# Kernel optimization log

Hardware: AMD Instinct MI355X
Metric: run time of the kernel (lower is better)

## Reference

```python
import jax, jax.numpy as jnp
import numpy as np

N_NODES = 10000
N_GRAPHS = 64
NEG_SLOPE = 0.2
EPS = 1e-16


def gat_conv(x, src, dst, W, a_src, a_dst, bias, heads, out_ch, num_nodes):
    """PyG GATConv (shared lin, add_self_loops already applied to src/dst)."""
    xl = (x @ W).reshape(num_nodes, heads, out_ch)          # [N,H,C]
    alpha_s = jnp.einsum('nhc,hc->nh', xl, a_src)           # [N,H]
    alpha_d = jnp.einsum('nhc,hc->nh', xl, a_dst)           # [N,H]
    e = jax.nn.leaky_relu(alpha_s[src] + alpha_d[dst], NEG_SLOPE)  # [E,H]
    # segment softmax over incoming edges of each destination node
    emax = jax.ops.segment_max(e, dst, num_segments=num_nodes)
    emax = jnp.where(jnp.isfinite(emax), emax, 0.0)
    ee = jnp.exp(e - emax[dst])
    denom = jax.ops.segment_sum(ee, dst, num_segments=num_nodes)
    alpha = ee / (denom[dst] + EPS)                         # [E,H]
    msg = xl[src] * alpha[:, :, None]                       # [E,H,C]
    out = jax.ops.segment_sum(msg, dst, num_segments=num_nodes)  # [N,H,C]
    return out.reshape(num_nodes, heads * out_ch) + bias


def setup_inputs() -> dict:
    key = jax.random.key(0)
    ks = jax.random.split(key, 16)
    H, C, IN = 8, 128, 128
    x = jax.random.normal(ks[0], (N_NODES, IN), jnp.float32)
    edge_index = jax.random.randint(ks[1], (2, 320000), 0, N_NODES, jnp.int64)
    batch = jnp.sort(jax.random.randint(ks[2], (N_NODES,), 0, N_GRAPHS, jnp.int64))
    g = lambda k, shp, fan: jax.random.normal(k, shp, jnp.float32) * (1.0 / np.sqrt(fan))
    return {
        'x': x, 'edge_index': edge_index, 'batch': batch,
        'W1': g(ks[3], (IN, H * C), IN),
        'a_src1': g(ks[4], (H, C), C), 'a_dst1': g(ks[5], (H, C), C),
        'b1': jnp.zeros((H * C,), jnp.float32),
        'W2': g(ks[6], (H * C, C), H * C),
        'a_src2': g(ks[7], (1, C), C), 'a_dst2': g(ks[8], (1, C), C),
        'b2': jnp.zeros((C,), jnp.float32),
        'lin1_w': g(ks[9], (C, 128), C), 'lin1_b': jnp.zeros((128,), jnp.float32),
        'lin2_w': g(ks[10], (128, 1), 128), 'lin2_b': jnp.zeros((1,), jnp.float32),
    }


def reference(x, edge_index, batch, W1, a_src1, a_dst1, b1, W2, a_src2, a_dst2, b2,
              lin1_w, lin1_b, lin2_w, lin2_b):
    loops = jnp.arange(N_NODES, dtype=edge_index.dtype)
    src = jnp.concatenate([edge_index[0], loops])
    dst = jnp.concatenate([edge_index[1], loops])
    h = jax.nn.elu(gat_conv(x, src, dst, W1, a_src1, a_dst1, b1, 8, 128, N_NODES))
    h = jax.nn.elu(gat_conv(h, src, dst, W2, a_src2, a_dst2, b2, 1, 128, N_NODES))
    # global mean pool over graphs
    sums = jax.ops.segment_sum(h, batch, num_segments=N_GRAPHS)
    cnts = jax.ops.segment_sum(jnp.ones((N_NODES,), h.dtype), batch, num_segments=N_GRAPHS)
    pooled = sums / jnp.maximum(cnts, 1.0)[:, None]         # [G,128]
    z = jax.nn.relu(pooled @ lin1_w + lin1_b)
    return (z @ lin2_w + lin2_b).squeeze(1)                 # [G]
```

## Files before the change

kernel.cpp:

```cpp
#include <hip/hip_runtime.h>
#include <math.h>

#define N_NODES 10000
#define N_GRAPHS 64
#define E_RAW 320000
#define E_ALL (E_RAW + N_NODES)
#define NEG_SLOPE 0.2f
#define EPS 1e-16f
#define CAP 192

typedef unsigned short ushort_t;
typedef short short8 __attribute__((ext_vector_type(8)));
typedef float floatx4 __attribute__((ext_vector_type(4)));

static __device__ __forceinline__ float bfl(unsigned u) {
  union { unsigned u; float f; } v; v.u = u << 16; return v.f;
}
static __device__ __forceinline__ float bfh(unsigned u) {
  union { unsigned u; float f; } v; v.u = u & 0xFFFF0000u; return v.f;
}
static __device__ __forceinline__ ushort_t f2bf(float f) {
  union { float f; unsigned u; } v; v.f = f;
  unsigned r = v.u + 0x7FFFu + ((v.u >> 16) & 1u);
  return (ushort_t)(r >> 16);
}

static __device__ __forceinline__ void load16_lds(const ushort_t* gp, ushort_t* ldsbase, int lane) {
#if __has_builtin(__builtin_amdgcn_global_load_lds)
  __builtin_amdgcn_global_load_lds((const __attribute__((address_space(1))) void*)gp,
                                   (__attribute__((address_space(3))) void*)ldsbase, 16, 0, 0);
#else
  *(uint4*)(ldsbase + lane * 8) = *(const uint4*)gp;
#endif
}

static __device__ __forceinline__ void swz_one(const float* __restrict__ W,
                                               ushort_t* __restrict__ Wsw,
                                               int idx, int K, int N) {
  int NT = N >> 4;
  int lane = idx & 63, tile = idx >> 6;
  int nt = tile % NT, kt = tile / NT;
  int n = nt * 16 + (lane & 15);
  int kb = kt * 32 + (lane >> 4) * 8;
  ushort4 lo, hi;
  lo.x = f2bf(W[(size_t)(kb + 0) * N + n]); lo.y = f2bf(W[(size_t)(kb + 1) * N + n]);
  lo.z = f2bf(W[(size_t)(kb + 2) * N + n]); lo.w = f2bf(W[(size_t)(kb + 3) * N + n]);
  hi.x = f2bf(W[(size_t)(kb + 4) * N + n]); hi.y = f2bf(W[(size_t)(kb + 5) * N + n]);
  hi.z = f2bf(W[(size_t)(kb + 6) * N + n]); hi.w = f2bf(W[(size_t)(kb + 7) * N + n]);
  *(ushort4*)(Wsw + (size_t)idx * 8) = lo;
  *(ushort4*)(Wsw + (size_t)idx * 8 + 4) = hi;
}

__global__ __launch_bounds__(1024) void prep_k(const float* __restrict__ x,
                                               const int* __restrict__ batch,
                                               const float* __restrict__ W1,
                                               const float* __restrict__ W2,
                                               ushort_t* __restrict__ xb,
                                               ushort_t* __restrict__ W1sw,
                                               ushort_t* __restrict__ W2sw,
                                               float* __restrict__ zero0,
                                               int* __restrict__ poolcnt) {
  __shared__ int shm[N_GRAPHS];
  const int b = blockIdx.x, t = threadIdx.x;
  if (b < 49) {
    int i4 = b * 1024 + t;
    if (i4 < 49548) *(float4*)(zero0 + i4 * 4) = make_float4(0.f, 0.f, 0.f, 0.f);
  } else if (b == 49) {
    if (t < N_GRAPHS) shm[t] = 0;
    __syncthreads();
    for (int n = t; n < N_NODES; n += 1024) atomicAdd(&shm[batch[n]], 1);
    __syncthreads();
    if (t < N_GRAPHS) poolcnt[t] = shm[t];
  } else if (b < 363) {
    int i4 = (b - 50) * 1024 + t;
    if (i4 < 320000) {
      float4 v = *(const float4*)(x + (size_t)i4 * 4);
      ushort4 o;
      o.x = f2bf(v.x); o.y = f2bf(v.y); o.z = f2bf(v.z); o.w = f2bf(v.w);
      *(ushort4*)(xb + (size_t)i4 * 4) = o;
    }
  } else if (b < 379) {
    int idx = (b - 363) * 1024 + t;
    if (idx < 16384) swz_one(W1, W1sw, idx, 128, 1024);
  } else {
    int idx = (b - 379) * 1024 + t;
    if (idx < 16384) swz_one(W2, W2sw, idx, 1024, 128);
  }
}

__global__ __launch_bounds__(256) void g1f_k(const ushort_t* __restrict__ A,
                                             const ushort_t* __restrict__ Bsw,
                                             ushort_t* __restrict__ Cb,
                                             const float* __restrict__ aS,
                                             const float* __restrict__ aD,
                                             float* __restrict__ asO,
                                             float* __restrict__ adO,
                                             const int* __restrict__ ei,
                                             int* __restrict__ degc,
                                             int* __restrict__ csr) {
  __shared__ ushort_t Albuf[32 * 512];
  __shared__ float epi[4][16][68];
  const int bid = blockIdx.x, t = threadIdx.x;
  if (bid >= 632) {
    int e = (bid - 632) * 256 + t;
    if (e < E_ALL) {
      int s, d;
      if (e < E_RAW) { s = ei[e]; d = ei[E_RAW + e]; }
      else           { s = d = e - E_RAW; }
      int pos = atomicAdd(&degc[d], 1);
      if (pos < CAP) csr[d * CAP + pos] = s;
    }
    return;
  }
  const int M = N_NODES, K = 128, NT = 64;
  const int lane = t & 63, w = t >> 6;
  const int wm = w >> 1, wn = w & 1;
  const int m0 = (bid >> 3) * 128;
  const int n0 = (bid & 7) * 128;
  const int g = lane >> 4, l16 = lane & 15;

  #pragma unroll
  for (int i = 0; i < 8; i++) {
    int tile = w * 8 + i;
    int mtl = tile >> 2, kt = tile & 3;
    int r = m0 + mtl * 16 + l16; r = r < M ? r : M - 1;
    load16_lds(A + (size_t)r * K + kt * 32 + g * 8, &Albuf[tile * 512], lane);
  }
  __syncthreads();

  floatx4 acc[4][4] = {};
  #pragma unroll
  for (int kt = 0; kt < 4; kt++) {
    short8 a[4], b[4];
    #pragma unroll
    for (int mi = 0; mi < 4; mi++)
      a[mi] = *(const short8*)&Albuf[(((wm * 4 + mi) * 4 + kt) * 64 + lane) * 8];
    #pragma unroll
    for (int ni = 0; ni < 4; ni++) {
      int nt = (n0 >> 4) + wn * 4 + ni;
      b[ni] = *(const short8*)(Bsw + ((size_t)(kt * NT + nt) * 64 + lane) * 8);
    }
    #pragma unroll
    for (int mi = 0; mi < 4; mi++)
      #pragma unroll
      for (int ni = 0; ni < 4; ni++)
        acc[mi][ni] = __builtin_amdgcn_mfma_f32_16x16x32_bf16(a[mi], b[ni], acc[mi][ni], 0, 0, 0);
  }

  const int h = bid & 7;
  const int r = lane >> 2, c0 = (lane & 3) * 16;
  const int colh = wn * 64 + c0;
  float asc[16], adc[16];
  #pragma unroll
  for (int c = 0; c < 16; c++) { asc[c] = aS[h * 128 + colh + c]; adc[c] = aD[h * 128 + colh + c]; }
  #pragma unroll
  for (int mi = 0; mi < 4; mi++) {
    #pragma unroll
    for (int ni = 0; ni < 4; ni++)
      #pragma unroll
      for (int reg = 0; reg < 4; reg++)
        epi[w][g * 4 + reg][ni * 16 + l16] = acc[mi][ni][reg];
    float4 v0 = *(float4*)&epi[w][r][c0];
    float4 v1 = *(float4*)&epi[w][r][c0 + 4];
    float4 v2 = *(float4*)&epi[w][r][c0 + 8];
    float4 v3 = *(float4*)&epi[w][r][c0 + 12];
    float vr[16] = {v0.x,v0.y,v0.z,v0.w, v1.x,v1.y,v1.z,v1.w,
                    v2.x,v2.y,v2.z,v2.w, v3.x,v3.y,v3.z,v3.w};
    int grow = m0 + wm * 64 + mi * 16 + r;
    float sp = 0.f, dp = 0.f;
    ushort_t hv[16];
    #pragma unroll
    for (int c = 0; c < 16; c++) {
      sp = fmaf(vr[c], asc[c], sp);
      dp = fmaf(vr[c], adc[c], dp);
      hv[c] = f2bf(vr[c]);
    }
    sp += __shfl_xor(sp, 1); sp += __shfl_xor(sp, 2);
    dp += __shfl_xor(dp, 1); dp += __shfl_xor(dp, 2);
    if (grow < M) {
      uint4 u0, u1;
      u0.x = (unsigned)hv[0] | ((unsigned)hv[1] << 16);
      u0.y = (unsigned)hv[2] | ((unsigned)hv[3] << 16);
      u0.z = (unsigned)hv[4] | ((unsigned)hv[5] << 16);
      u0.w = (unsigned)hv[6] | ((unsigned)hv[7] << 16);
      u1.x = (unsigned)hv[8] | ((unsigned)hv[9] << 16);
      u1.y = (unsigned)hv[10] | ((unsigned)hv[11] << 16);
      u1.z = (unsigned)hv[12] | ((unsigned)hv[13] << 16);
      u1.w = (unsigned)hv[14] | ((unsigned)hv[15] << 16);
      ushort_t* cp = Cb + (size_t)grow * 1024 + (bid & 7) * 128 + wn * 64 + c0;
      *(uint4*)cp = u0;
      *(uint4*)(cp + 8) = u1;
      if ((lane & 3) == 0) {
        atomicAdd(&asO[grow * 8 + h], sp);
        atomicAdd(&adO[grow * 8 + h], dp);
      }
    }
  }
}

__global__ __launch_bounds__(256) void gemm2_k(const ushort_t* __restrict__ A,
                                               const ushort_t* __restrict__ Bsw,
                                               ushort_t* __restrict__ Cb,
                                               const float* __restrict__ aS,
                                               const float* __restrict__ aD,
                                               float* __restrict__ asO,
                                               float* __restrict__ adO) {
  const int M = N_NODES, K = 1024, NT = 8;
  __shared__ ushort_t Albuf[8 * 512];
  __shared__ float epi[4][16][68];
  const int t = threadIdx.x, lane = t & 63, w = t >> 6;
  const int wm = w >> 1, wn = w & 1;
  const int mb0 = blockIdx.x * 32;
  const int g = lane >> 4, l16 = lane & 15;

  floatx4 acc[4] = {};
  for (int ch = 0; ch < 8; ch++) {
    #pragma unroll
    for (int i = 0; i < 2; i++) {
      int tile = w * 2 + i;
      int mtl = tile >> 2, kt = tile & 3;
      int r = mb0 + mtl * 16 + l16; r = r < M ? r : M - 1;
      load16_lds(A + (size_t)r * K + (ch * 4 + kt) * 32 + g * 8, &Albuf[tile * 512], lane);
    }
    __syncthreads();
    #pragma unroll
    for (int ks = 0; ks < 4; ks++) {
      short8 a = *(const short8*)&Albuf[(((wm * 4 + ks)) * 64 + lane) * 8];
      #pragma unroll
      for (int ni = 0; ni < 4; ni++) {
        int nt = wn * 4 + ni, ktg = ch * 4 + ks;
        short8 b = *(const short8*)(Bsw + ((size_t)(ktg * NT + nt) * 64 + lane) * 8);
        acc[ni] = __builtin_amdgcn_mfma_f32_16x16x32_bf16(a, b, acc[ni], 0, 0, 0);
      }
    }
    __syncthreads();
  }

  const int r = lane >> 2, c0 = (lane & 3) * 16;
  const int colh = wn * 64 + c0;
  float asc[16], adc[16];
  #pragma unroll
  for (int c = 0; c < 16; c++) { asc[c] = aS[colh + c]; adc[c] = aD[colh + c]; }
  #pragma unroll
  for (int ni = 0; ni < 4; ni++)
    #pragma unroll
    for (int reg = 0; reg < 4; reg++)
      epi[w][g * 4 + reg][ni * 16 + l16] = acc[ni][reg];
  float4 v0 = *(float4*)&epi[w][r][c0];
  float4 v1 = *(float4*)&epi[w][r][c0 + 4];
  float4 v2 = *(float4*)&epi[w][r][c0 + 8];
  float4 v3 = *(float4*)&epi[w][r][c0 + 12];
  float vr[16] = {v0.x,v0.y,v0.z,v0.w, v1.x,v1.y,v1.z,v1.w,
                  v2.x,v2.y,v2.z,v2.w, v3.x,v3.y,v3.z,v3.w};
  int grow = mb0 + wm * 16 + r;
  float sp = 0.f, dp = 0.f;
  ushort_t hv[16];
  #pragma unroll
  for (int c = 0; c < 16; c++) {
    sp = fmaf(vr[c], asc[c], sp);
    dp = fmaf(vr[c], adc[c], dp);
    hv[c] = f2bf(vr[c]);
  }
  sp += __shfl_xor(sp, 1); sp += __shfl_xor(sp, 2);
  dp += __shfl_xor(dp, 1); dp += __shfl_xor(dp, 2);
  if (grow < M) {
    uint4 u0, u1;
    u0.x = (unsigned)hv[0] | ((unsigned)hv[1] << 16);
    u0.y = (unsigned)hv[2] | ((unsigned)hv[3] << 16);
    u0.z = (unsigned)hv[4] | ((unsigned)hv[5] << 16);
    u0.w = (unsigned)hv[6] | ((unsigned)hv[7] << 16);
    u1.x = (unsigned)hv[8] | ((unsigned)hv[9] << 16);
    u1.y = (unsigned)hv[10] | ((unsigned)hv[11] << 16);
    u1.z = (unsigned)hv[12] | ((unsigned)hv[13] << 16);
    u1.w = (unsigned)hv[14] | ((unsigned)hv[15] << 16);
    ushort_t* cp = Cb + (size_t)grow * 128 + colh;
    *(uint4*)cp = u0;
    *(uint4*)(cp + 8) = u1;
    if ((lane & 3) == 0) {
      atomicAdd(&asO[grow], sp);
      atomicAdd(&adO[grow], dp);
    }
  }
}

__global__ __launch_bounds__(128) void agg1_k(const ushort_t* __restrict__ xlb,
                                              const float* __restrict__ as1,
                                              const float* __restrict__ ad1,
                                              const float* __restrict__ b1,
                                              const int* __restrict__ degc,
                                              const int* __restrict__ csr,
                                              ushort_t* __restrict__ out) {
  int dst = blockIdx.x, t = threadIdx.x;
  int deg = degc[dst]; deg = deg < CAP ? deg : CAP;
  int beg = dst * CAP;
  __shared__ int ss[CAP];
  __shared__ float alE[CAP][8];
  __shared__ float sred[8][17];
  __shared__ float mh[8], sh[8];
  for (int e = t; e < deg; e += 128) ss[e] = csr[beg + e];
  __syncthreads();
  int h2 = t & 7, slot = t >> 3;
  float adh2 = ad1[dst * 8 + h2];
  float pm = -1e30f;
  for (int e = slot; e < deg; e += 16) {
    float v = as1[ss[e] * 8 + h2] + adh2;
    v = v > 0.f ? v : NEG_SLOPE * v;
    alE[e][h2] = v;
    pm = fmaxf(pm, v);
  }
  sred[h2][slot] = pm;
  __syncthreads();
  if (t < 8) {
    float m = sred[t][0];
    for (int i = 1; i < 16; i++) m = fmaxf(m, sred[t][i]);
    mh[t] = m;
  }
  __syncthreads();
  float m2 = mh[h2];
  float ps = 0.f;
  for (int e = slot; e < deg; e += 16) ps += __expf(alE[e][h2] - m2);
  sred[h2][slot] = ps;
  __syncthreads();
  if (t < 8) {
    float s = 0.f;
    for (int i = 0; i < 16; i++) s += sred[t][i];
    sh[t] = 1.0f / (s + EPS);
  }
  __syncthreads();
  float inv2 = sh[h2];
  for (int e = slot; e < deg; e += 16) alE[e][h2] = __expf(alE[e][h2] - m2) * inv2;
  __syncthreads();
  int h = t >> 4;
  float acc[8] = {};
  const ushort_t* xp = xlb + 8 * t;
  #pragma unroll 4
  for (int e = 0; e < deg; e++) {
    float a = alE[e][h];
    const uint4 u = *(const uint4*)(xp + (size_t)ss[e] * 1024);
    acc[0] = fmaf(a, bfl(u.x), acc[0]); acc[1] = fmaf(a, bfh(u.x), acc[1]);
    acc[2] = fmaf(a, bfl(u.y), acc[2]); acc[3] = fmaf(a, bfh(u.y), acc[3]);
    acc[4] = fmaf(a, bfl(u.z), acc[4]); acc[5] = fmaf(a, bfh(u.z), acc[5]);
    acc[6] = fmaf(a, bfl(u.w), acc[6]); acc[7] = fmaf(a, bfh(u.w), acc[7]);
  }
  ushort_t hv[8];
  #pragma unroll
  for (int j = 0; j < 8; j++) {
    int o = 8 * t + j;
    float v = acc[j] + b1[o];
    v = v > 0.f ? v : (expf(v) - 1.0f);
    hv[j] = f2bf(v);
  }
  uint4 up;
  up.x = (unsigned)hv[0] | ((unsigned)hv[1] << 16);
  up.y = (unsigned)hv[2] | ((unsigned)hv[3] << 16);
  up.z = (unsigned)hv[4] | ((unsigned)hv[5] << 16);
  up.w = (unsigned)hv[6] | ((unsigned)hv[7] << 16);
  *(uint4*)(out + (size_t)dst * 1024 + 8 * t) = up;
}

__global__ __launch_bounds__(64) void agg2_k(const ushort_t* __restrict__ xlb2,
                                             const float* __restrict__ as2,
                                             const float* __restrict__ ad2,
                                             const float* __restrict__ b2,
                                             const int* __restrict__ degc,
                                             const int* __restrict__ csr,
                                             const int* __restrict__ batch,
                                             float* __restrict__ poolsum) {
  int dst = blockIdx.x, t = threadIdx.x;
  int deg = degc[dst]; deg = deg < CAP ? deg : CAP;
  int beg = dst * CAP;
  float adv = ad2[dst];
  __shared__ int ss[CAP];
  __shared__ float al[CAP];
  for (int e = t; e < deg; e += 64) ss[e] = csr[beg + e];
  __syncthreads();
  float pm = -1e30f;
  for (int e = t; e < deg; e += 64) {
    float v = as2[ss[e]] + adv;
    v = v > 0.f ? v : NEG_SLOPE * v;
    al[e] = v;
    pm = fmaxf(pm, v);
  }
  #pragma unroll
  for (int off = 32; off; off >>= 1) pm = fmaxf(pm, __shfl_xor(pm, off));
  float m = pm;
  float ps = 0.f;
  for (int e = t; e < deg; e += 64) ps += __expf(al[e] - m);
  #pragma unroll
  for (int off = 32; off; off >>= 1) ps += __shfl_xor(ps, off);
  float inv = 1.0f / (ps + EPS);
  for (int e = t; e < deg; e += 64) al[e] = __expf(al[e] - m) * inv;
  __syncthreads();
  float acc0 = 0.f, acc1 = 0.f;
  const ushort_t* xp = xlb2 + 2 * t;
  #pragma unroll 4
  for (int e = 0; e < deg; e++) {
    unsigned u = *(const unsigned*)(xp + (size_t)ss[e] * 128);
    acc0 = fmaf(al[e], bfl(u), acc0);
    acc1 = fmaf(al[e], bfh(u), acc1);
  }
  int c0 = 2 * t;
  float v0 = acc0 + b2[c0];
  float v1 = acc1 + b2[c0 + 1];
  v0 = v0 > 0.f ? v0 : (expf(v0) - 1.0f);
  v1 = v1 > 0.f ? v1 : (expf(v1) - 1.0f);
  int g = batch[dst];
  atomicAdd(&poolsum[g * 128 + c0], v0);
  atomicAdd(&poolsum[g * 128 + c0 + 1], v1);
}

__global__ __launch_bounds__(128) void final_k(const float* __restrict__ poolsum,
                                               const int* __restrict__ cnt,
                                               const float* __restrict__ l1w,
                                               const float* __restrict__ l1b,
                                               const float* __restrict__ l2w,
                                               const float* __restrict__ l2b,
                                               float* __restrict__ out) {
  int g = blockIdx.x, t = threadIdx.x;
  __shared__ float pooled[128];
  float c = fmaxf((float)cnt[g], 1.0f);
  pooled[t] = poolsum[g * 128 + t] / c;
  __syncthreads();
  float acc = l1b[t];
  for (int i = 0; i < 128; i++) acc = fmaf(pooled[i], l1w[i * 128 + t], acc);
  acc = fmaxf(acc, 0.0f);
  float p = acc * l2w[t];
  #pragma unroll
  for (int off = 32; off; off >>= 1) p += __shfl_down(p, off);
  __shared__ float r[2];
  if ((t & 63) == 0) r[t >> 6] = p;
  __syncthreads();
  if (t == 0) out[g] = r[0] + r[1] + l2b[0];
}

extern "C" void kernel_launch(void* const* d_in, const int* in_sizes, int n_in,
                              void* d_out, int out_size, void* d_ws, size_t ws_size,
                              hipStream_t stream) {
  const float* x    = (const float*)d_in[0];
  const int*   ei   = (const int*)d_in[1];
  const int*   batch= (const int*)d_in[2];
  const float* W1   = (const float*)d_in[3];
  const float* aS1  = (const float*)d_in[4];
  const float* aD1  = (const float*)d_in[5];
  const float* b1   = (const float*)d_in[6];
  const float* W2   = (const float*)d_in[7];
  const float* aS2  = (const float*)d_in[8];
  const float* aD2  = (const float*)d_in[9];
  const float* b2   = (const float*)d_in[10];
  const float* l1w  = (const float*)d_in[11];
  const float* l1b  = (const float*)d_in[12];
  const float* l2w  = (const float*)d_in[13];
  const float* l2b  = (const float*)d_in[14];
  float* out = (float*)d_out;

  ushort_t* xlb1   = (ushort_t*)d_ws;
  ushort_t* h1b    = xlb1 + 10240000;
  ushort_t* xlb2   = h1b + 10240000;
  ushort_t* xb     = xlb2 + 1280000;
  ushort_t* W1sw   = xb + 1280000;
  ushort_t* W2sw   = W1sw + 131072;
  float*    zero0  = (float*)(W2sw + 131072);
  float*    as1    = zero0;
  float*    ad1    = as1 + 80000;
  float*    as2    = ad1 + 80000;
  float*    ad2    = as2 + 10000;
  float*    poolsum= ad2 + 10000;
  int*      degc   = (int*)(poolsum + 8192);
  int*      poolcnt= degc + 10000;
  int*      csr    = poolcnt + 64;

  prep_k<<<395, 1024, 0, stream>>>(x, batch, W1, W2, xb, W1sw, W2sw, zero0, poolcnt);
  g1f_k<<<632 + 1290, 256, 0, stream>>>(xb, W1sw, xlb1, aS1, aD1, as1, ad1, ei, degc, csr);
  agg1_k<<<N_NODES, 128, 0, stream>>>(xlb1, as1, ad1, b1, degc, csr, h1b);
  gemm2_k<<<313, 256, 0, stream>>>(h1b, W2sw, xlb2, aS2, aD2, as2, ad2);
  agg2_k<<<N_NODES, 64, 0, stream>>>(xlb2, as2, ad2, b2, degc, csr, batch, poolsum);
  final_k<<<N_GRAPHS, 128, 0, stream>>>(poolsum, poolcnt, l1w, l1b, l2w, l2b, out);
}
```

Baseline: 259.5 us.

## Fuse all stages into one persistent kernel with software grid barriers

Replaces six kernel launches with one persistent kernel of 512 blocks that runs prep, GEMM1, aggregation 1, GEMM2, aggregation 2 and the final MLP in sequence, separated by atomic-counter grid barriers. Zeroing moves to a hipMemsetAsync. Aggregation blocks now handle two or four destination nodes each, so all stages fit in a fixed 256-thread block. This removes launch gaps and tail effects between stages. In exchange it assumes all 512 blocks are co-resident (a deadlock risk otherwise), adds barrier spin cost, and gives up the per-kernel block shapes and occupancy tuning.

```diff
diff --git a/kernel.cpp b/kernel.cpp
--- a/kernel.cpp
+++ b/kernel.cpp
@@ -8,6 +8,7 @@
 #define NEG_SLOPE 0.2f
 #define EPS 1e-16f
 #define CAP 192
+#define NBLK 512
 
 typedef unsigned short ushort_t;
 typedef short short8 __attribute__((ext_vector_type(8)));
@@ -51,74 +52,29 @@
   *(ushort4*)(Wsw + (size_t)idx * 8 + 4) = hi;
 }
 
-__global__ __launch_bounds__(1024) void prep_k(const float* __restrict__ x,
-                                               const int* __restrict__ batch,
-                                               const float* __restrict__ W1,
-                                               const float* __restrict__ W2,
-                                               ushort_t* __restrict__ xb,
-                                               ushort_t* __restrict__ W1sw,
-                                               ushort_t* __restrict__ W2sw,
-                                               float* __restrict__ zero0,
-                                               int* __restrict__ poolcnt) {
-  __shared__ int shm[N_GRAPHS];
-  const int b = blockIdx.x, t = threadIdx.x;
-  if (b < 49) {
-    int i4 = b * 1024 + t;
-    if (i4 < 49548) *(float4*)(zero0 + i4 * 4) = make_float4(0.f, 0.f, 0.f, 0.f);
-  } else if (b == 49) {
-    if (t < N_GRAPHS) shm[t] = 0;
-    __syncthreads();
-    for (int n = t; n < N_NODES; n += 1024) atomicAdd(&shm[batch[n]], 1);
-    __syncthreads();
-    if (t < N_GRAPHS) poolcnt[t] = shm[t];
-  } else if (b < 363) {
-    int i4 = (b - 50) * 1024 + t;
-    if (i4 < 320000) {
-      float4 v = *(const float4*)(x + (size_t)i4 * 4);
-      ushort4 o;
-      o.x = f2bf(v.x); o.y = f2bf(v.y); o.z = f2bf(v.z); o.w = f2bf(v.w);
-      *(ushort4*)(xb + (size_t)i4 * 4) = o;
-    }
-  } else if (b < 379) {
-    int idx = (b - 363) * 1024 + t;
-    if (idx < 16384) swz_one(W1, W1sw, idx, 128, 1024);
-  } else {
-    int idx = (b - 379) * 1024 + t;
-    if (idx < 16384) swz_one(W2, W2sw, idx, 1024, 128);
-  }
-}
-
-__global__ __launch_bounds__(256) void g1f_k(const ushort_t* __restrict__ A,
-                                             const ushort_t* __restrict__ Bsw,
-                                             ushort_t* __restrict__ Cb,
-                                             const float* __restrict__ aS,
-                                             const float* __restrict__ aD,
-                                             float* __restrict__ asO,
-                                             float* __restrict__ adO,
-                                             const int* __restrict__ ei,
-                                             int* __restrict__ degc,
-                                             int* __restrict__ csr) {
-  __shared__ ushort_t Albuf[32 * 512];
-  __shared__ float epi[4][16][68];
-  const int bid = blockIdx.x, t = threadIdx.x;
-  if (bid >= 632) {
-    int e = (bid - 632) * 256 + t;
-    if (e < E_ALL) {
-      int s, d;
-      if (e < E_RAW) { s = ei[e]; d = ei[E_RAW + e]; }
-      else           { s = d = e - E_RAW; }
-      int pos = atomicAdd(&degc[d], 1);
-      if (pos < CAP) csr[d * CAP + pos] = s;
-    }
-    return;
-  }
+static __device__ __forceinline__ void gbar(int* cnt) {
+  __syncthreads();
+  if (threadIdx.x == 0) {
+    __hip_atomic_fetch_add(cnt, 1, __ATOMIC_ACQ_REL, __HIP_MEMORY_SCOPE_AGENT);
+    while (__hip_atomic_load(cnt, __ATOMIC_ACQUIRE, __HIP_MEMORY_SCOPE_AGENT) < NBLK)
+      __builtin_amdgcn_s_sleep(2);
+  }
+  __syncthreads();
+}
+
+static __device__ __forceinline__ void gemm1_tile(int v, char* shraw,
+    const ushort_t* __restrict__ A, const ushort_t* __restrict__ Bsw,
+    ushort_t* __restrict__ Cb, const float* __restrict__ aS,
+    const float* __restrict__ aD, float* __restrict__ asO, float* __restrict__ adO) {
+  ushort_t* Albuf = (ushort_t*)shraw;
+  float (*epi)[16][68] = (float (*)[16][68])shraw;
+  const int t = threadIdx.x, lane = t & 63, w = t >> 6;
+  const int wm = w >> 1, wn = w & 1;
+  const int m0 = (v >> 3) * 128;
+  const int h = v & 7;
+  const int g = lane >> 4, l16 = lane & 15;
   const int M = N_NODES, K = 128, NT = 64;
-  const int lane = t & 63, w = t >> 6;
-  const int wm = w >> 1, wn = w & 1;
-  const int m0 = (bid >> 3) * 128;
-  const int n0 = (bid & 7) * 128;
-  const int g = lane >> 4, l16 = lane & 15;
-
+  __syncthreads();
   #pragma unroll
   for (int i = 0; i < 8; i++) {
     int tile = w * 8 + i;
@@ -127,7 +83,6 @@
     load16_lds(A + (size_t)r * K + kt * 32 + g * 8, &Albuf[tile * 512], lane);
   }
   __syncthreads();
-
   floatx4 acc[4][4] = {};
   #pragma unroll
   for (int kt = 0; kt < 4; kt++) {
@@ -137,7 +92,7 @@
       a[mi] = *(const short8*)&Albuf[(((wm * 4 + mi) * 4 + kt) * 64 + lane) * 8];
     #pragma unroll
     for (int ni = 0; ni < 4; ni++) {
-      int nt = (n0 >> 4) + wn * 4 + ni;
+      int nt = h * 8 + wn * 4 + ni;
       b[ni] = *(const short8*)(Bsw + ((size_t)(kt * NT + nt) * 64 + lane) * 8);
     }
     #pragma unroll
@@ -146,8 +101,7 @@
       for (int ni = 0; ni < 4; ni++)
         acc[mi][ni] = __builtin_amdgcn_mfma_f32_16x16x32_bf16(a[mi], b[ni], acc[mi][ni], 0, 0, 0);
   }
-
-  const int h = bid & 7;
+  __syncthreads();
   const int r = lane >> 2, c0 = (lane & 3) * 16;
   const int colh = wn * 64 + c0;
   float asc[16], adc[16];
@@ -187,7 +141,7 @@
       u1.y = (unsigned)hv[10] | ((unsigned)hv[11] << 16);
       u1.z = (unsigned)hv[12] | ((unsigned)hv[13] << 16);
       u1.w = (unsigned)hv[14] | ((unsigned)hv[15] << 16);
-      ushort_t* cp = Cb + (size_t)grow * 1024 + (bid & 7) * 128 + wn * 64 + c0;
+      ushort_t* cp = Cb + (size_t)grow * 1024 + h * 128 + wn * 64 + c0;
       *(uint4*)cp = u0;
       *(uint4*)(cp + 8) = u1;
       if ((lane & 3) == 0) {
@@ -198,21 +152,17 @@
   }
 }
 
-__global__ __launch_bounds__(256) void gemm2_k(const ushort_t* __restrict__ A,
-                                               const ushort_t* __restrict__ Bsw,
-                                               ushort_t* __restrict__ Cb,
-                                               const float* __restrict__ aS,
-                                               const float* __restrict__ aD,
-                                               float* __restrict__ asO,
-                                               float* __restrict__ adO) {
-  const int M = N_NODES, K = 1024, NT = 8;
-  __shared__ ushort_t Albuf[8 * 512];
-  __shared__ float epi[4][16][68];
+static __device__ __forceinline__ void gemm2_tile(int v, char* shraw,
+    const ushort_t* __restrict__ A, const ushort_t* __restrict__ Bsw,
+    ushort_t* __restrict__ Cb, const float* __restrict__ aS,
+    const float* __restrict__ aD, float* __restrict__ asO, float* __restrict__ adO) {
+  ushort_t* Albuf = (ushort_t*)shraw;
+  float (*epi)[16][68] = (float (*)[16][68])(shraw + 8192);
   const int t = threadIdx.x, lane = t & 63, w = t >> 6;
   const int wm = w >> 1, wn = w & 1;
-  const int mb0 = blockIdx.x * 32;
+  const int mb0 = v * 32;
   const int g = lane >> 4, l16 = lane & 15;
-
+  const int M = N_NODES, K = 1024, NT = 8;
   floatx4 acc[4] = {};
   for (int ch = 0; ch < 8; ch++) {
     #pragma unroll
@@ -235,7 +185,6 @@
     }
     __syncthreads();
   }
-
   const int r = lane >> 2, c0 = (lane & 3) * 16;
   const int colh = wn * 64 + c0;
   float asc[16], adc[16];
@@ -281,62 +230,60 @@
       atomicAdd(&adO[grow], dp);
     }
   }
-}
-
-__global__ __launch_bounds__(128) void agg1_k(const ushort_t* __restrict__ xlb,
-                                              const float* __restrict__ as1,
-                                              const float* __restrict__ ad1,
-                                              const float* __restrict__ b1,
-                                              const int* __restrict__ degc,
-                                              const int* __restrict__ csr,
-                                              ushort_t* __restrict__ out) {
-  int dst = blockIdx.x, t = threadIdx.x;
+  __syncthreads();
+}
+
+static __device__ __forceinline__ void agg1_pair(int p, char* shraw,
+    const ushort_t* __restrict__ xlb, const float* __restrict__ as1,
+    const float* __restrict__ ad1, const float* __restrict__ b1,
+    const int* __restrict__ degc, const int* __restrict__ csr,
+    ushort_t* __restrict__ out) {
+  struct Sh { int ss[CAP]; float alE[CAP][8]; float sred[8][17]; float mh[8]; float sh[8]; };
+  const int t = threadIdx.x, half = t >> 7, th = t & 127;
+  Sh* S = ((Sh*)shraw) + half;
+  const int dst = 2 * p + half;
   int deg = degc[dst]; deg = deg < CAP ? deg : CAP;
-  int beg = dst * CAP;
-  __shared__ int ss[CAP];
-  __shared__ float alE[CAP][8];
-  __shared__ float sred[8][17];
-  __shared__ float mh[8], sh[8];
-  for (int e = t; e < deg; e += 128) ss[e] = csr[beg + e];
-  __syncthreads();
-  int h2 = t & 7, slot = t >> 3;
+  const int beg = dst * CAP;
+  for (int e = th; e < deg; e += 128) S->ss[e] = csr[beg + e];
+  __syncthreads();
+  const int h2 = th & 7, slot = th >> 3;
   float adh2 = ad1[dst * 8 + h2];
   float pm = -1e30f;
   for (int e = slot; e < deg; e += 16) {
-    float v = as1[ss[e] * 8 + h2] + adh2;
+    float v = as1[S->ss[e] * 8 + h2] + adh2;
     v = v > 0.f ? v : NEG_SLOPE * v;
-    alE[e][h2] = v;
+    S->alE[e][h2] = v;
     pm = fmaxf(pm, v);
   }
-  sred[h2][slot] = pm;
-  __syncthreads();
-  if (t < 8) {
-    float m = sred[t][0];
-    for (int i = 1; i < 16; i++) m = fmaxf(m, sred[t][i]);
-    mh[t] = m;
-  }
-  __syncthreads();
-  float m2 = mh[h2];
+  S->sred[h2][slot] = pm;
+  __syncthreads();
+  if (th < 8) {
+    float m = S->sred[th][0];
+    for (int i = 1; i < 16; i++) m = fmaxf(m, S->sred[th][i]);
+    S->mh[th] = m;
+  }
+  __syncthreads();
+  float m2 = S->mh[h2];
   float ps = 0.f;
-  for (int e = slot; e < deg; e += 16) ps += __expf(alE[e][h2] - m2);
-  sred[h2][slot] = ps;
-  __syncthreads();
-  if (t < 8) {
+  for (int e = slot; e < deg; e += 16) ps += __expf(S->alE[e][h2] - m2);
+  S->sred[h2][slot] = ps;
+  __syncthreads();
+  if (th < 8) {
     float s = 0.f;
-    for (int i = 0; i < 16; i++) s += sred[t][i];
-    sh[t] = 1.0f / (s + EPS);
-  }
-  __syncthreads();
-  float inv2 = sh[h2];
-  for (int e = slot; e < deg; e += 16) alE[e][h2] = __expf(alE[e][h2] - m2) * inv2;
-  __syncthreads();
-  int h = t >> 4;
+    for (int i = 0; i < 16; i++) s += S->sred[th][i];
+    S->sh[th] = 1.0f / (s + EPS);
+  }
+  __syncthreads();
+  float inv2 = S->sh[h2];
+  for (int e = slot; e < deg; e += 16) S->alE[e][h2] = __expf(S->alE[e][h2] - m2) * inv2;
+  __syncthreads();
+  const int h = th >> 4;
   float acc[8] = {};
-  const ushort_t* xp = xlb + 8 * t;
+  const ushort_t* xp = xlb + 8 * th;
   #pragma unroll 4
   for (int e = 0; e < deg; e++) {
-    float a = alE[e][h];
-    const uint4 u = *(const uint4*)(xp + (size_t)ss[e] * 1024);
+    float a = S->alE[e][h];
+    const uint4 u = *(const uint4*)(xp + (size_t)S->ss[e] * 1024);
     acc[0] = fmaf(a, bfl(u.x), acc[0]); acc[1] = fmaf(a, bfh(u.x), acc[1]);
     acc[2] = fmaf(a, bfl(u.y), acc[2]); acc[3] = fmaf(a, bfh(u.y), acc[3]);
     acc[4] = fmaf(a, bfl(u.z), acc[4]); acc[5] = fmaf(a, bfh(u.z), acc[5]);
@@ -345,7 +292,7 @@
   ushort_t hv[8];
   #pragma unroll
   for (int j = 0; j < 8; j++) {
-    int o = 8 * t + j;
+    int o = 8 * th + j;
     float v = acc[j] + b1[o];
     v = v > 0.f ? v : (expf(v) - 1.0f);
     hv[j] = f2bf(v);
@@ -355,51 +302,48 @@
   up.y = (unsigned)hv[2] | ((unsigned)hv[3] << 16);
   up.z = (unsigned)hv[4] | ((unsigned)hv[5] << 16);
   up.w = (unsigned)hv[6] | ((unsigned)hv[7] << 16);
-  *(uint4*)(out + (size_t)dst * 1024 + 8 * t) = up;
-}
-
-__global__ __launch_bounds__(64) void agg2_k(const ushort_t* __restrict__ xlb2,
-                                             const float* __restrict__ as2,
-                                             const float* __restrict__ ad2,
-                                             const float* __restrict__ b2,
-                                             const int* __restrict__ degc,
-                                             const int* __restrict__ csr,
-                                             const int* __restrict__ batch,
-                                             float* __restrict__ poolsum) {
-  int dst = blockIdx.x, t = threadIdx.x;
+  *(uint4*)(out + (size_t)dst * 1024 + 8 * th) = up;
+  __syncthreads();
+}
+
+static __device__ __forceinline__ void agg2_quad(int q, char* shraw,
+    const ushort_t* __restrict__ xlb2, const float* __restrict__ as2,
+    const float* __restrict__ ad2, const float* __restrict__ b2,
+    const int* __restrict__ degc, const int* __restrict__ csr,
+    const int* __restrict__ batch, float* __restrict__ poolsum) {
+  struct Sh { int ss[CAP]; float al[CAP]; };
+  const int t = threadIdx.x, qt = t >> 6, l = t & 63;
+  Sh* S = ((Sh*)shraw) + qt;
+  const int dst = 4 * q + qt;
   int deg = degc[dst]; deg = deg < CAP ? deg : CAP;
-  int beg = dst * CAP;
+  const int beg = dst * CAP;
   float adv = ad2[dst];
-  __shared__ int ss[CAP];
-  __shared__ float al[CAP];
-  for (int e = t; e < deg; e += 64) ss[e] = csr[beg + e];
-  __syncthreads();
+  for (int e = l; e < deg; e += 64) S->ss[e] = csr[beg + e];
   float pm = -1e30f;
-  for (int e = t; e < deg; e += 64) {
-    float v = as2[ss[e]] + adv;
+  for (int e = l; e < deg; e += 64) {
+    float v = as2[S->ss[e]] + adv;
     v = v > 0.f ? v : NEG_SLOPE * v;
-    al[e] = v;
+    S->al[e] = v;
     pm = fmaxf(pm, v);
   }
   #pragma unroll
   for (int off = 32; off; off >>= 1) pm = fmaxf(pm, __shfl_xor(pm, off));
   float m = pm;
   float ps = 0.f;
-  for (int e = t; e < deg; e += 64) ps += __expf(al[e] - m);
+  for (int e = l; e < deg; e += 64) ps += __expf(S->al[e] - m);
   #pragma unroll
   for (int off = 32; off; off >>= 1) ps += __shfl_xor(ps, off);
   float inv = 1.0f / (ps + EPS);
-  for (int e = t; e < deg; e += 64) al[e] = __expf(al[e] - m) * inv;
-  __syncthreads();
+  for (int e = l; e < deg; e += 64) S->al[e] = __expf(S->al[e] - m) * inv;
   float acc0 = 0.f, acc1 = 0.f;
-  const ushort_t* xp = xlb2 + 2 * t;
+  const ushort_t* xp = xlb2 + 2 * l;
   #pragma unroll 4
   for (int e = 0; e < deg; e++) {
-    unsigned u = *(const unsigned*)(xp + (size_t)ss[e] * 128);
-    acc0 = fmaf(al[e], bfl(u), acc0);
-    acc1 = fmaf(al[e], bfh(u), acc1);
-  }
-  int c0 = 2 * t;
+    unsigned u = *(const unsigned*)(xp + (size_t)S->ss[e] * 128);
+    acc0 = fmaf(S->al[e], bfl(u), acc0);
+    acc1 = fmaf(S->al[e], bfh(u), acc1);
+  }
+  int c0 = 2 * l;
   float v0 = acc0 + b2[c0];
   float v1 = acc1 + b2[c0 + 1];
   v0 = v0 > 0.f ? v0 : (expf(v0) - 1.0f);
@@ -409,28 +353,85 @@
   atomicAdd(&poolsum[g * 128 + c0 + 1], v1);
 }
 
-__global__ __launch_bounds__(128) void final_k(const float* __restrict__ poolsum,
-                                               const int* __restrict__ cnt,
-                                               const float* __restrict__ l1w,
-                                               const float* __restrict__ l1b,
-                                               const float* __restrict__ l2w,
-                                               const float* __restrict__ l2b,
-                                               float* __restrict__ out) {
-  int g = blockIdx.x, t = threadIdx.x;
-  __shared__ float pooled[128];
+static __device__ __forceinline__ void final_half(char* shraw,
+    const float* __restrict__ poolsum, const int* __restrict__ cnt,
+    const float* __restrict__ l1w, const float* __restrict__ l1b,
+    const float* __restrict__ l2w, const float* __restrict__ l2b,
+    float* __restrict__ out) {
+  struct Sh { float pooled[128]; float r[2]; };
+  const int t = threadIdx.x, half = t >> 7, th = t & 127;
+  Sh* F = ((Sh*)shraw) + half;
+  const int g = blockIdx.x * 2 + half;
   float c = fmaxf((float)cnt[g], 1.0f);
-  pooled[t] = poolsum[g * 128 + t] / c;
-  __syncthreads();
-  float acc = l1b[t];
-  for (int i = 0; i < 128; i++) acc = fmaf(pooled[i], l1w[i * 128 + t], acc);
+  F->pooled[th] = poolsum[g * 128 + th] / c;
+  __syncthreads();
+  float acc = l1b[th];
+  for (int i = 0; i < 128; i++) acc = fmaf(F->pooled[i], l1w[i * 128 + th], acc);
   acc = fmaxf(acc, 0.0f);
-  float p = acc * l2w[t];
+  float p = acc * l2w[th];
   #pragma unroll
   for (int off = 32; off; off >>= 1) p += __shfl_down(p, off);
-  __shared__ float r[2];
-  if ((t & 63) == 0) r[t >> 6] = p;
-  __syncthreads();
-  if (t == 0) out[g] = r[0] + r[1] + l2b[0];
+  if ((th & 63) == 0) F->r[th >> 6] = p;
+  __syncthreads();
+  if (th == 0) out[g] = F->r[0] + F->r[1] + l2b[0];
+}
+
+__global__ __launch_bounds__(256, 2) void mega_k(
+    const float* __restrict__ x, const int* __restrict__ ei,
+    const int* __restrict__ batch,
+    const float* __restrict__ W1, const float* __restrict__ aS1,
+    const float* __restrict__ aD1, const float* __restrict__ b1,
+    const float* __restrict__ W2, const float* __restrict__ aS2,
+    const float* __restrict__ aD2, const float* __restrict__ b2,
+    const float* __restrict__ l1w, const float* __restrict__ l1b,
+    const float* __restrict__ l2w, const float* __restrict__ l2b,
+    ushort_t* xb, ushort_t* W1sw, ushort_t* W2sw,
+    ushort_t* xlb1, ushort_t* h1b, ushort_t* xlb2,
+    float* as1, float* ad1, float* as2, float* ad2,
+    float* poolsum, int* poolcnt, int* degc, int* csr, int* bar,
+    float* out) {
+  __shared__ __align__(16) char shraw[32768];
+  const int bid = blockIdx.x, t = threadIdx.x;
+  const int gtid = bid * 256 + t;
+
+  for (int i4 = gtid; i4 < 320000; i4 += NBLK * 256) {
+    float4 v = *(const float4*)(x + (size_t)i4 * 4);
+    ushort4 o;
+    o.x = f2bf(v.x); o.y = f2bf(v.y); o.z = f2bf(v.z); o.w = f2bf(v.w);
+    *(ushort4*)(xb + (size_t)i4 * 4) = o;
+  }
+  for (int idx = gtid; idx < 32768; idx += NBLK * 256) {
+    if (idx < 16384) swz_one(W1, W1sw, idx, 128, 1024);
+    else             swz_one(W2, W2sw, idx - 16384, 1024, 128);
+  }
+  for (int n = gtid; n < N_NODES; n += NBLK * 256) atomicAdd(&poolcnt[batch[n]], 1);
+  for (int e = gtid; e < E_ALL; e += NBLK * 256) {
+    int s, d;
+    if (e < E_RAW) { s = ei[e]; d = ei[E_RAW + e]; }
+    else           { s = d = e - E_RAW; }
+    int pos = atomicAdd(&degc[d], 1);
+    if (pos < CAP) csr[d * CAP + pos] = s;
+  }
+  gbar(&bar[0]);
+
+  for (int v = bid; v < 632; v += NBLK)
+    gemm1_tile(v, shraw, xb, W1sw, xlb1, aS1, aD1, as1, ad1);
+  gbar(&bar[1]);
+
+  for (int p = bid; p < 5000; p += NBLK)
+    agg1_pair(p, shraw, xlb1, as1, ad1, b1, degc, csr, h1b);
+  gbar(&bar[2]);
+
+  for (int v = bid; v < 313; v += NBLK)
+    gemm2_tile(v, shraw, h1b, W2sw, xlb2, aS2, aD2, as2, ad2);
+  gbar(&bar[3]);
+
+  for (int q = bid; q < 2500; q += NBLK)
+    agg2_quad(q, shraw, xlb2, as2, ad2, b2, degc, csr, batch, poolsum);
+  gbar(&bar[4]);
+
+  if (bid < 32)
+    final_half(shraw, poolsum, poolcnt, l1w, l1b, l2w, l2b, out);
 }
 
 extern "C" void kernel_launch(void* const* d_in, const int* in_sizes, int n_in,
@@ -467,12 +468,15 @@
   float*    poolsum= ad2 + 10000;
   int*      degc   = (int*)(poolsum + 8192);
   int*      poolcnt= degc + 10000;
-  int*      csr    = poolcnt + 64;
-
-  prep_k<<<395, 1024, 0, stream>>>(x, batch, W1, W2, xb, W1sw, W2sw, zero0, poolcnt);
-  g1f_k<<<632 + 1290, 256, 0, stream>>>(xb, W1sw, xlb1, aS1, aD1, as1, ad1, ei, degc, csr);
-  agg1_k<<<N_NODES, 128, 0, stream>>>(xlb1, as1, ad1, b1, degc, csr, h1b);
-  gemm2_k<<<313, 256, 0, stream>>>(h1b, W2sw, xlb2, aS2, aD2, as2, ad2);
-  agg2_k<<<N_NODES, 64, 0, stream>>>(xlb2, as2, ad2, b2, degc, csr, batch, poolsum);
-  final_k<<<N_GRAPHS, 128, 0, stream>>>(poolsum, poolcnt, l1w, l1b, l2w, l2b, out);
-}
+  int*      bar    = poolcnt + 64;
+  int*      csr    = bar + 8;
+
+  size_t zero_words = 80000 + 80000 + 10000 + 10000 + 8192 + 10000 + 64 + 8;
+  hipMemsetAsync(zero0, 0, zero_words * 4, stream);
+
+  mega_k<<<NBLK, 256, 0, stream>>>(x, ei, batch, W1, aS1, aD1, b1, W2, aS2, aD2, b2,
+                                   l1w, l1b, l2w, l2b,
+                                   xb, W1sw, W2sw, xlb1, h1b, xlb2,
+                                   as1, ad1, as2, ad2, poolsum, poolcnt, degc, csr, bar,
+                                   out);
+}
```

Result: slower. 865.1 us (+233.4%).

## Split layer-1 aggregation into one 64-thread block per (node, head)

Applied to the files above, without the earlier changes.

The layer-1 GAT aggregation kernel now launches one single-wavefront block per destination node and head instead of one 128-thread block per node. Softmax reductions use wavefront shuffles instead of shared-memory reductions and multiple barriers. Each lane gathers 4-byte bf16 pairs rather than 16-byte vectors. This exposes eight times more blocks and removes barriers, but it repeats the CSR index loads per head and uses narrower, less efficient gathers.

```diff
diff --git a/kernel.cpp b/kernel.cpp
--- a/kernel.cpp
+++ b/kernel.cpp
@@ -283,79 +283,54 @@
   }
 }
 
-__global__ __launch_bounds__(128) void agg1_k(const ushort_t* __restrict__ xlb,
-                                              const float* __restrict__ as1,
-                                              const float* __restrict__ ad1,
-                                              const float* __restrict__ b1,
-                                              const int* __restrict__ degc,
-                                              const int* __restrict__ csr,
-                                              ushort_t* __restrict__ out) {
-  int dst = blockIdx.x, t = threadIdx.x;
+__global__ __launch_bounds__(64) void agg1_k(const ushort_t* __restrict__ xlb,
+                                             const float* __restrict__ as1,
+                                             const float* __restrict__ ad1,
+                                             const float* __restrict__ b1,
+                                             const int* __restrict__ degc,
+                                             const int* __restrict__ csr,
+                                             ushort_t* __restrict__ out) {
+  const int bid = blockIdx.x, t = threadIdx.x;
+  const int h = bid & 7, dst = bid >> 3;
   int deg = degc[dst]; deg = deg < CAP ? deg : CAP;
-  int beg = dst * CAP;
+  const int beg = dst * CAP;
   __shared__ int ss[CAP];
-  __shared__ float alE[CAP][8];
-  __shared__ float sred[8][17];
-  __shared__ float mh[8], sh[8];
-  for (int e = t; e < deg; e += 128) ss[e] = csr[beg + e];
-  __syncthreads();
-  int h2 = t & 7, slot = t >> 3;
-  float adh2 = ad1[dst * 8 + h2];
+  __shared__ float al[CAP];
+  for (int e = t; e < deg; e += 64) ss[e] = csr[beg + e];
+  __syncthreads();
+  float adh = ad1[dst * 8 + h];
   float pm = -1e30f;
-  for (int e = slot; e < deg; e += 16) {
-    float v = as1[ss[e] * 8 + h2] + adh2;
+  for (int e = t; e < deg; e += 64) {
+    float v = as1[ss[e] * 8 + h] + adh;
     v = v > 0.f ? v : NEG_SLOPE * v;
-    alE[e][h2] = v;
+    al[e] = v;
     pm = fmaxf(pm, v);
   }
-  sred[h2][slot] = pm;
-  __syncthreads();
-  if (t < 8) {
-    float m = sred[t][0];
-    for (int i = 1; i < 16; i++) m = fmaxf(m, sred[t][i]);
-    mh[t] = m;
-  }
-  __syncthreads();
-  float m2 = mh[h2];
+  #pragma unroll
+  for (int off = 32; off; off >>= 1) pm = fmaxf(pm, __shfl_xor(pm, off));
   float ps = 0.f;
-  for (int e = slot; e < deg; e += 16) ps += __expf(alE[e][h2] - m2);
-  sred[h2][slot] = ps;
-  __syncthreads();
-  if (t < 8) {
-    float s = 0.f;
-    for (int i = 0; i < 16; i++) s += sred[t][i];
-    sh[t] = 1.0f / (s + EPS);
-  }
-  __syncthreads();
-  float inv2 = sh[h2];
-  for (int e = slot; e < deg; e += 16) alE[e][h2] = __expf(alE[e][h2] - m2) * inv2;
-  __syncthreads();
-  int h = t >> 4;
-  float acc[8] = {};
-  const ushort_t* xp = xlb + 8 * t;
+  __syncthreads();
+  for (int e = t; e < deg; e += 64) ps += __expf(al[e] - pm);
+  #pragma unroll
+  for (int off = 32; off; off >>= 1) ps += __shfl_xor(ps, off);
+  float inv = 1.0f / (ps + EPS);
+  for (int e = t; e < deg; e += 64) al[e] = __expf(al[e] - pm) * inv;
+  __syncthreads();
+  const ushort_t* xp = xlb + h * 128 + 2 * t;
+  float acc0 = 0.f, acc1 = 0.f;
   #pragma unroll 4
   for (int e = 0; e < deg; e++) {
-    float a = alE[e][h];
-    const uint4 u = *(const uint4*)(xp + (size_t)ss[e] * 1024);
-    acc[0] = fmaf(a, bfl(u.x), acc[0]); acc[1] = fmaf(a, bfh(u.x), acc[1]);
-    acc[2] = fmaf(a, bfl(u.y), acc[2]); acc[3] = fmaf(a, bfh(u.y), acc[3]);
-    acc[4] = fmaf(a, bfl(u.z), acc[4]); acc[5] = fmaf(a, bfh(u.z), acc[5]);
-    acc[6] = fmaf(a, bfl(u.w), acc[6]); acc[7] = fmaf(a, bfh(u.w), acc[7]);
-  }
-  ushort_t hv[8];
-  #pragma unroll
-  for (int j = 0; j < 8; j++) {
-    int o = 8 * t + j;
-    float v = acc[j] + b1[o];
-    v = v > 0.f ? v : (expf(v) - 1.0f);
-    hv[j] = f2bf(v);
-  }
-  uint4 up;
-  up.x = (unsigned)hv[0] | ((unsigned)hv[1] << 16);
-  up.y = (unsigned)hv[2] | ((unsigned)hv[3] << 16);
-  up.z = (unsigned)hv[4] | ((unsigned)hv[5] << 16);
-  up.w = (unsigned)hv[6] | ((unsigned)hv[7] << 16);
-  *(uint4*)(out + (size_t)dst * 1024 + 8 * t) = up;
+    unsigned u = *(const unsigned*)(xp + (size_t)ss[e] * 1024);
+    acc0 = fmaf(al[e], bfl(u), acc0);
+    acc1 = fmaf(al[e], bfh(u), acc1);
+  }
+  int o = h * 128 + 2 * t;
+  float v0 = acc0 + b1[o];
+  float v1 = acc1 + b1[o + 1];
+  v0 = v0 > 0.f ? v0 : (expf(v0) - 1.0f);
+  v1 = v1 > 0.f ? v1 : (expf(v1) - 1.0f);
+  unsigned up = (unsigned)f2bf(v0) | ((unsigned)f2bf(v1) << 16);
+  *(unsigned*)(out + (size_t)dst * 1024 + o) = up;
 }
 
 __global__ __launch_bounds__(64) void agg2_k(const ushort_t* __restrict__ xlb2,
@@ -471,7 +446,7 @@
 
   prep_k<<<395, 1024, 0, stream>>>(x, batch, W1, W2, xb, W1sw, W2sw, zero0, poolcnt);
   g1f_k<<<632 + 1290, 256, 0, stream>>>(xb, W1sw, xlb1, aS1, aD1, as1, ad1, ei, degc, csr);
-  agg1_k<<<N_NODES, 128, 0, stream>>>(xlb1, as1, ad1, b1, degc, csr, h1b);
+  agg1_k<<<N_NODES * 8, 64, 0, stream>>>(xlb1, as1, ad1, b1, degc, csr, h1b);
   gemm2_k<<<313, 256, 0, stream>>>(h1b, W2sw, xlb2, aS2, aD2, as2, ad2);
   agg2_k<<<N_NODES, 64, 0, stream>>>(xlb2, as2, ad2, b2, degc, csr, batch, poolsum);
   final_k<<<N_GRAPHS, 128, 0, stream>>>(poolsum, poolcnt, l1w, l1b, l2w, l2b, out);
```

Measured after the change: 233.9 us. 9.8% less time.
